# Optimization experiments

Measured on AMD Instinct MI355X. Metric: run time of the kernel, lower is better.

Reference implementation:

```python
import jax, jax.numpy as jnp
import numpy as np

N_HEAD = 16
BLOCK_SIZE = 2049  # w2 last dim = block_size - 1 = 2048


def setup_inputs() -> dict:
    key = jax.random.key(0)
    ks = jax.random.split(key, 9)
    B, T, C = 2, 2048, 1024
    hd = C // N_HEAD
    M = BLOCK_SIZE - 1
    return {
        "x": jax.random.normal(ks[0], (B, T, C), jnp.float32),
        "w1_w": jax.random.normal(ks[1], (C, C), jnp.float32) * 0.02,
        "w1_b": jax.random.normal(ks[2], (C,), jnp.float32) * 0.02,
        # torch uniform_(a=-0.001, b=0.001)
        "w2": jax.random.uniform(ks[3], (N_HEAD, hd, M), jnp.float32, -0.001, 0.001),
        "b2": jax.random.normal(ks[4], (M,), jnp.float32) * 0.02,
        "value_w": jax.random.normal(ks[5], (C, C), jnp.float32) * 0.02,
        "value_b": jax.random.normal(ks[6], (C,), jnp.float32) * 0.02,
        "proj_w": jax.random.normal(ks[7], (C, C), jnp.float32) * 0.02,
        "proj_b": jax.random.normal(ks[8], (C,), jnp.float32) * 0.02,
    }


def reference(x, w1_w, w1_b, w2, b2, value_w, value_b, proj_w, proj_b):
    B, T, C = x.shape
    H = N_HEAD
    hd = C // H
    M = w2.shape[-1]  # block_size - 1
    # kernel = relu(w1(x)), split heads -> [B, H, T, hd]
    k = jax.nn.relu(x @ w1_w.T + w1_b).reshape(B, T, H, hd).transpose(0, 2, 1, 3)
    # synthesizer scores: [B, H, T, M]
    attn = jnp.einsum('bhtd,hdm->bhtm', k, w2) + b2
    # causal mask = tril(ones(block,block))[:T, :M] == 0 -> -inf
    causal = jnp.tril(jnp.ones((T, M), dtype=bool))
    attn = jnp.where(causal, attn, -jnp.inf)
    # softmax over first T score columns
    attn = jax.nn.softmax(attn[..., :T], axis=-1)  # [B, H, T, T]
    v = (x @ value_w.T + value_b).reshape(B, T, H, hd).transpose(0, 2, 1, 3)
    out = jnp.einsum('bhts,bhsd->bhtd', attn, v)
    out = out.transpose(0, 2, 1, 3).reshape(B, T, C)
    return out @ proj_w.T + proj_b
```

## Files before the change

### kernel.cpp

```cpp
#include <hip/hip_runtime.h>
#include <math.h>
#include <stdint.h>

typedef __bf16 bf16;
typedef __bf16 bf16x8 __attribute__((ext_vector_type(8)));
typedef __bf16 bf16x4 __attribute__((ext_vector_type(4)));
typedef float f32x4 __attribute__((ext_vector_type(4)));
typedef float f32x16 __attribute__((ext_vector_type(16)));
typedef unsigned int u32;

__device__ __forceinline__ int swz(int row, int chunk) {
    return row * 64 + ((chunk ^ (row & 7)) << 3);
}

__device__ __forceinline__ void gld16(void* lds, const void* g) {
    __builtin_amdgcn_global_load_lds(
        (const __attribute__((address_space(1))) u32*)g,
        (__attribute__((address_space(3))) u32*)lds, 16, 0, 0);
}

__global__ void cast_bf16_k(const float* __restrict__ src, bf16* __restrict__ dst, int n) {
    const int stride = gridDim.x * blockDim.x * 4;
    for (int i = (blockIdx.x * blockDim.x + threadIdx.x) * 4; i < n; i += stride) {
        float4 v = *(const float4*)(src + i);
        bf16x4 o = {(bf16)v.x, (bf16)v.y, (bf16)v.z, (bf16)v.w};
        *(bf16x4*)(dst + i) = o;
    }
}

__global__ void cast3_bf16_k(const float* __restrict__ s0, bf16* __restrict__ d0,
                             const float* __restrict__ s1, bf16* __restrict__ d1,
                             const float* __restrict__ s2, bf16* __restrict__ d2, int n) {
    const int stride = gridDim.x * blockDim.x * 4;
    for (int i = (blockIdx.x * blockDim.x + threadIdx.x) * 4; i < n; i += stride) {
        float4 v0 = *(const float4*)(s0 + i);
        float4 v1 = *(const float4*)(s1 + i);
        float4 v2 = *(const float4*)(s2 + i);
        bf16x4 o0 = {(bf16)v0.x, (bf16)v0.y, (bf16)v0.z, (bf16)v0.w};
        bf16x4 o1 = {(bf16)v1.x, (bf16)v1.y, (bf16)v1.z, (bf16)v1.w};
        bf16x4 o2 = {(bf16)v2.x, (bf16)v2.y, (bf16)v2.z, (bf16)v2.w};
        *(bf16x4*)(d0 + i) = o0;
        *(bf16x4*)(d1 + i) = o1;
        *(bf16x4*)(d2 + i) = o2;
    }
}

__global__ __launch_bounds__(256) void w2_transpose_k(const float* __restrict__ w2,
                                                      bf16* __restrict__ w2t, int M) {
    __shared__ float Tf[64][65];
    const int h = blockIdx.y, m0 = blockIdx.x * 64, t = threadIdx.x;
    {
        const int dr = t >> 4, c4 = (t & 15) * 4;
        #pragma unroll
        for (int it = 0; it < 4; ++it) {
            const int d = dr + it * 16;
            float4 v = *(const float4*)(w2 + ((size_t)h * 64 + d) * M + m0 + c4);
            Tf[d][c4] = v.x; Tf[d][c4 + 1] = v.y; Tf[d][c4 + 2] = v.z; Tf[d][c4 + 3] = v.w;
        }
    }
    __syncthreads();
    const int m = t >> 2;
    #pragma unroll
    for (int it = 0; it < 2; ++it) {
        const int ch = (t & 3) + it * 4;
        bf16x8 o;
        #pragma unroll
        for (int j = 0; j < 8; ++j) o[j] = (bf16)Tf[ch * 8 + j][m];
        *(bf16x8*)(w2t + ((size_t)h * M + m0 + m) * 64 + ch * 8) = o;
    }
}

__global__ __launch_bounds__(256, 2) void gemm_bf16_k(const bf16* __restrict__ A,
                                                   const bf16* __restrict__ Bw,
                                                   const float* __restrict__ bias,
                                                   const float* __restrict__ bias2,
                                                   float* __restrict__ C0,
                                                   bf16* __restrict__ CK,
                                                   bf16* __restrict__ CV,
                                                   int M, int N, int K, int mode, int Ns)
{
    __shared__ __align__(16) bf16 As[2][128 * 64];
    __shared__ __align__(16) bf16 Bs[2][128 * 64];
    const int tid = threadIdx.x;
    const int w = tid >> 6, l = tid & 63;
    const int wr = w >> 1, wc = w & 1;
    const int lc = l & 15, lg = l >> 4;
    const int row0 = blockIdx.y * 128, col0 = blockIdx.x * 128;

    f32x4 acc[4][4] = {};

    const int nk = K >> 6;
    auto issue = [&](int buf, int k0) {
        #pragma unroll
        for (int i = 0; i < 4; ++i) {
            const int br = (w * 4 + i) * 8;
            const int r = br + (l >> 3);
            const int gs = (l & 7) ^ (r & 7);
            gld16(&As[buf][br * 64], A  + (size_t)(row0 + r) * K + k0 + gs * 8);
            gld16(&Bs[buf][br * 64], Bw + (size_t)(col0 + r) * K + k0 + gs * 8);
        }
    };

    issue(0, 0);
    int cur = 0;
    for (int kt = 0; kt < nk; ++kt) {
        if (kt + 1 < nk) {
            issue(cur ^ 1, (kt + 1) << 6);
            asm volatile("s_waitcnt vmcnt(8)" ::: "memory");
        } else {
            asm volatile("s_waitcnt vmcnt(0)" ::: "memory");
        }
        __builtin_amdgcn_s_barrier();
        #pragma unroll
        for (int ks = 0; ks < 2; ++ks) {
            bf16x8 af[4], bfv[4];
            #pragma unroll
            for (int i = 0; i < 4; ++i) {
                af[i]  = *(const bf16x8*)&As[cur][swz(wr * 64 + i * 16 + lc, ks * 4 + lg)];
                bfv[i] = *(const bf16x8*)&Bs[cur][swz(wc * 64 + i * 16 + lc, ks * 4 + lg)];
            }
            #pragma unroll
            for (int mi = 0; mi < 4; ++mi)
                #pragma unroll
                for (int ni = 0; ni < 4; ++ni)
                    acc[mi][ni] = __builtin_amdgcn_mfma_f32_16x16x32_bf16(af[mi], bfv[ni], acc[mi][ni], 0, 0, 0);
        }
        asm volatile("s_waitcnt lgkmcnt(0)" ::: "memory");
        __builtin_amdgcn_s_barrier();
        cur ^= 1;
    }

    #pragma unroll
    for (int ni = 0; ni < 4; ++ni) {
        const int col = col0 + wc * 64 + ni * 16 + lc;
        #pragma unroll
        for (int mi = 0; mi < 4; ++mi) {
            const int rowb = row0 + wr * 64 + mi * 16 + lg * 4;
            f32x4 v = acc[mi][ni];
            if (mode == 0) {
                const float bv = bias[col];
                #pragma unroll
                for (int r = 0; r < 4; ++r)
                    C0[(size_t)(rowb + r) * N + col] = v[r] + bv;
            } else if (col < Ns) {
                const float bv = bias[col];
                #pragma unroll
                for (int r = 0; r < 4; ++r)
                    CK[(size_t)(rowb + r) * Ns + col] = (bf16)fmaxf(v[r] + bv, 0.f);
            } else {
                const float bv = bias2[col - Ns];
                const int b = rowb >> 11, tt = rowb & 2047;
                bf16x4 o = {(bf16)(v[0] + bv), (bf16)(v[1] + bv),
                            (bf16)(v[2] + bv), (bf16)(v[3] + bv)};
                *(bf16x4*)(CV + ((size_t)b * Ns + (col - Ns)) * 2048 + tt) = o;
            }
        }
    }
}

__global__ __launch_bounds__(512, 4) void synth_attn_v11(const bf16* __restrict__ Kb,
                                                         const bf16* __restrict__ VT,
                                                         const bf16* __restrict__ w2t,
                                                         const float* __restrict__ b2,
                                                         bf16* __restrict__ Ob)
{
    constexpr int T = 2048, C = 1024, M = 2048;
    __shared__ __align__(16) bf16 ring[2][2][8192];
    __shared__ float b2l[M];
    const int tid = threadIdx.x;
    const int w = tid >> 6, l = tid & 63;
    const int c = l & 31, hi = l >> 5;
    const int sg = w & 1, qh = w >> 1;

    const int bx = blockIdx.x;
    const int u = bx & 255, rg = bx >> 8;
    const int t128 = rg ? (15 - (u & 15)) : (u & 15);
    const int bh = (u >> 4) + (rg << 4);
    const int h = bh & 15, b = bh >> 4;
    const int t0w = t128 * 128 + qh * 32;
    const int myT = 2 * t128 + (qh >> 1);

    *(float4*)&b2l[tid * 4] = *(const float4*)(b2 + tid * 4);
    __syncthreads();

    const bf16* Wg = w2t + (size_t)h * M * 64;
    const bf16* Vg = VT + ((size_t)b * C + h * 64) * T;

    const bf16* Kg = Kb + ((size_t)(b * T + t0w + c)) * C + h * 64 + hi * 8;
    bf16x8 kf[4];
    #pragma unroll
    for (int kst = 0; kst < 4; ++kst) kf[kst] = *(const bf16x8*)(Kg + kst * 16);

    auto stage = [&](int buf, int sb) {
        bf16* dst = &ring[sg][buf][0];
        const int s0 = sb * 64;
        const int jb = (qh & 1) * 4;
        if (qh < 2) {
            #pragma unroll
            for (int j = 0; j < 4; ++j) {
                const int jj = jb + j, r = jj >> 2, kst = jj & 3;
                gld16(dst + jj * 512,
                      Wg + ((size_t)(s0 + r * 32 + c)) * 64 + kst * 16 + hi * 8);
            }
        } else {
            #pragma unroll
            for (int j = 0; j < 4; ++j) {
                const int jj = jb + j, r = jj >> 2, m = jj & 3;
                gld16(dst + 4096 + jj * 512,
                      Vg + ((size_t)(r * 32 + c)) * T + s0 + m * 16 + hi * 8);
            }
        }
    };

    const int nIter = t128 + 1;
    stage(0, sg);

    f32x16 o0 = {}, o1 = {};
    float lsum = 0.f;

    for (int i = 0; i < nIter; ++i) {
        const int sb = 2 * i + sg;
        if (i + 1 < nIter) {
            stage((i + 1) & 1, sb + 2);
            asm volatile("s_waitcnt vmcnt(4)" ::: "memory");
        } else {
            asm volatile("s_waitcnt vmcnt(0)" ::: "memory");
        }
        __builtin_amdgcn_s_barrier();

        if (sb <= myT) {
            const bf16* Wb = &ring[sg][i & 1][0];
            const bf16* Vb = &ring[sg][i & 1][4096];
            const int s0 = sb * 64;

            f32x16 sv0, sv1;
            #pragma unroll
            for (int qd = 0; qd < 4; ++qd) {
                float4 b4 = *(const float4*)&b2l[s0 + qd * 8 + 4 * hi];
                float4 b5 = *(const float4*)&b2l[s0 + 32 + qd * 8 + 4 * hi];
                sv0[4*qd] = b4.x; sv0[4*qd+1] = b4.y; sv0[4*qd+2] = b4.z; sv0[4*qd+3] = b4.w;
                sv1[4*qd] = b5.x; sv1[4*qd+1] = b5.y; sv1[4*qd+2] = b5.z; sv1[4*qd+3] = b5.w;
            }
            #pragma unroll
            for (int kst = 0; kst < 4; ++kst) {
                bf16x8 w0 = *(const bf16x8*)&Wb[kst * 512 + l * 8];
                bf16x8 w1 = *(const bf16x8*)&Wb[(4 + kst) * 512 + l * 8];
                sv0 = __builtin_amdgcn_mfma_f32_32x32x16_bf16(w0, kf[kst], sv0, 0, 0, 0);
                sv1 = __builtin_amdgcn_mfma_f32_32x32x16_bf16(w1, kf[kst], sv1, 0, 0, 0);
            }

            const bool diag = (sb == myT);
            const int qv = (qh & 1) * 32 + c;
            u32 U0[8], U1[8];
            #pragma unroll
            for (int qd = 0; qd < 4; ++qd) {
                float e0[4], e1[4];
                #pragma unroll
                for (int k = 0; k < 4; ++k) {
                    const int sbase = qd * 8 + 4 * hi + k;
                    float ev0 = __expf(sv0[4*qd + k]);
                    float ev1 = __expf(sv1[4*qd + k]);
                    if (diag && sbase > qv)      ev0 = 0.f;
                    if (diag && sbase + 32 > qv) ev1 = 0.f;
                    lsum += ev0 + ev1;
                    e0[k] = ev0; e1[k] = ev1;
                }
                union { bf16x4 v; u32 uu[2]; } p0, p1;
                p0.v = {(bf16)e0[0], (bf16)e0[1], (bf16)e0[2], (bf16)e0[3]};
                p1.v = {(bf16)e1[0], (bf16)e1[1], (bf16)e1[2], (bf16)e1[3]};
                U0[2*qd] = p0.uu[0]; U0[2*qd+1] = p0.uu[1];
                U1[2*qd] = p1.uu[0]; U1[2*qd+1] = p1.uu[1];
            }

            #define PV_TILE(Uarr, st)                                              \
            {                                                                      \
                _Pragma("unroll")                                                  \
                for (int kk = 0; kk < 2; ++kk) {                                   \
                    u32 A00 = Uarr[4*kk],   A01 = Uarr[4*kk+1];                    \
                    u32 A10 = Uarr[4*kk+2], A11 = Uarr[4*kk+3];                    \
                    u32 s00 = (u32)__shfl_xor((int)A00, 32);                       \
                    u32 s01 = (u32)__shfl_xor((int)A01, 32);                       \
                    u32 s10 = (u32)__shfl_xor((int)A10, 32);                       \
                    u32 s11 = (u32)__shfl_xor((int)A11, 32);                       \
                    union { u32 uu[4]; bf16x8 v; } pa;                             \
                    pa.uu[0] = hi ? s10 : A00;                                     \
                    pa.uu[1] = hi ? s11 : A01;                                     \
                    pa.uu[2] = hi ? A10 : s00;                                     \
                    pa.uu[3] = hi ? A11 : s01;                                     \
                    const int m = (st) * 2 + kk;                                   \
                    bf16x8 v0 = *(const bf16x8*)&Vb[m * 512 + l * 8];              \
                    bf16x8 v1 = *(const bf16x8*)&Vb[(4 + m) * 512 + l * 8];        \
                    o0 = __builtin_amdgcn_mfma_f32_32x32x16_bf16(pa.v, v0, o0, 0, 0, 0); \
                    o1 = __builtin_amdgcn_mfma_f32_32x32x16_bf16(pa.v, v1, o1, 0, 0, 0); \
                }                                                                  \
            }
            PV_TILE(U0, 0)
            PV_TILE(U1, 1)
            #undef PV_TILE
        }

        asm volatile("s_waitcnt lgkmcnt(0)" ::: "memory");
        __builtin_amdgcn_s_barrier();
    }

    float* scr = (float*)&ring[0][0][0];
    float* base = scr + qh * 2112;
    if (sg == 1) {
        #pragma unroll
        for (int k = 0; k < 16; ++k) base[k * 64 + l] = o0[k];
        #pragma unroll
        for (int k = 0; k < 16; ++k) base[(16 + k) * 64 + l] = o1[k];
        base[32 * 64 + l] = lsum;
    }
    __syncthreads();
    if (sg == 0) {
        #pragma unroll
        for (int k = 0; k < 16; ++k) o0[k] += base[k * 64 + l];
        #pragma unroll
        for (int k = 0; k < 16; ++k) o1[k] += base[(16 + k) * 64 + l];
        lsum += base[32 * 64 + l];
        const float inv = 1.f / (lsum + __shfl_xor(lsum, 32));
        #pragma unroll
        for (int r = 0; r < 16; ++r) {
            const int q_ = (r & 3) + 8 * (r >> 2) + 4 * hi;
            const float iv = __shfl(inv, q_);
            bf16* dst = Ob + (size_t)(b * T + t0w + q_) * C + h * 64;
            dst[c]      = (bf16)(o0[r] * iv);
            dst[32 + c] = (bf16)(o1[r] * iv);
        }
    }
}

extern "C" void kernel_launch(void* const* d_in, const int* in_sizes, int n_in,
                              void* d_out, int out_size, void* d_ws, size_t ws_size,
                              hipStream_t stream) {
    const float* x       = (const float*)d_in[0];
    const float* w1_w    = (const float*)d_in[1];
    const float* w1_b    = (const float*)d_in[2];
    const float* w2      = (const float*)d_in[3];
    const float* b2      = (const float*)d_in[4];
    const float* value_w = (const float*)d_in[5];
    const float* value_b = (const float*)d_in[6];
    const float* proj_w  = (const float*)d_in[7];
    const float* proj_b  = (const float*)d_in[8];

    const int B = 2, T = 2048, C = 1024, H = 16, M = 2048;
    const int R = B * T;

    bf16* xb  = (bf16*)d_ws;
    bf16* w1b = xb  + (size_t)R * C;
    bf16* vwb = w1b + (size_t)C * C;
    bf16* w2t = vwb + (size_t)C * C;
    bf16* pwb = w2t + (size_t)H * M * 64;
    bf16* Kb  = pwb + (size_t)C * C;
    bf16* VTb = Kb  + (size_t)R * C;
    bf16* Ob  = VTb + (size_t)R * C;

    cast_bf16_k<<<1024, 256, 0, stream>>>(x, xb, R * C);
    cast3_bf16_k<<<512, 256, 0, stream>>>(w1_w, w1b, value_w, vwb, proj_w, pwb, C * C);
    w2_transpose_k<<<dim3(M / 64, H), 256, 0, stream>>>(w2, w2t, M);

    gemm_bf16_k<<<dim3(2 * C / 128, R / 128), 256, 0, stream>>>(
        xb, w1b, w1_b, value_b, nullptr, Kb, VTb, R, 2 * C, C, 1, C);

    synth_attn_v11<<<dim3(512), 512, 0, stream>>>(Kb, VTb, w2t, b2, Ob);

    gemm_bf16_k<<<dim3(C / 128, R / 128), 256, 0, stream>>>(
        Ob, pwb, proj_b, nullptr, (float*)d_out, nullptr, nullptr, R, C, C, 0, C);
}
```

Baseline: 109.9 us.

## Split attention over key-range chunks with atomic accumulation and separate normalize pass

Replaces the 512-thread blocks, which covered each query tile's full causal key range split between two wave groups, with 256-thread blocks that each handle up to 8 key tiles of one query tile. Later query tiles get more blocks, giving 1280 roughly balanced blocks. Partial outputs and row sums are combined with float atomicAdds into zeroed fp32 buffers, and a new kernel normalizes them and casts to bf16. The aim is better load balance and occupancy under the causal triangle. The cost is a memset, heavy global atomic traffic, an extra full-size fp32 read/write pass, and non-deterministic summation order.

```diff
diff --git a/kernel.cpp b/kernel.cpp
--- a/kernel.cpp
+++ b/kernel.cpp
@@ -158,30 +158,35 @@
     }
 }
 
-__global__ __launch_bounds__(512, 4) void synth_attn_v11(const bf16* __restrict__ Kb,
+__global__ __launch_bounds__(256, 4) void synth_attn_v12(const bf16* __restrict__ Kb,
                                                          const bf16* __restrict__ VT,
                                                          const bf16* __restrict__ w2t,
                                                          const float* __restrict__ b2,
-                                                         bf16* __restrict__ Ob)
+                                                         float* __restrict__ Oacc,
+                                                         float* __restrict__ Lacc)
 {
-    constexpr int T = 2048, C = 1024, M = 2048;
-    __shared__ __align__(16) bf16 ring[2][2][8192];
-    __shared__ float b2l[M];
+    constexpr int T = 2048, C = 1024, M = 2048, H = 16;
+    __shared__ __align__(16) bf16 ring[2][8192];
+    __shared__ float b2l[512];
     const int tid = threadIdx.x;
     const int w = tid >> 6, l = tid & 63;
     const int c = l & 31, hi = l >> 5;
-    const int sg = w & 1, qh = w >> 1;
 
     const int bx = blockIdx.x;
-    const int u = bx & 255, rg = bx >> 8;
-    const int t128 = rg ? (15 - (u & 15)) : (u & 15);
-    const int bh = (u >> 4) + (rg << 4);
+    const int bh = bx / 40, u = bx % 40;
+    int t, sp;
+    if (u < 4)       { t = u;                sp = 0; }
+    else if (u < 12) { t = 4 + ((u - 4) >> 1);  sp = (u - 4) & 1; }
+    else if (u < 24) { t = 8 + (u - 12) / 3;    sp = (u - 12) % 3; }
+    else             { t = 12 + ((u - 24) >> 2); sp = (u - 24) & 3; }
     const int h = bh & 15, b = bh >> 4;
-    const int t0w = t128 * 128 + qh * 32;
-    const int myT = 2 * t128 + (qh >> 1);
-
-    *(float4*)&b2l[tid * 4] = *(const float4*)(b2 + tid * 4);
-    __syncthreads();
+    const int t0w = t * 128 + w * 32;
+    const int myT = 2 * t + (w >> 1);
+    const int sLo = sp * 8;
+    const int nT = min(8, 2 * t + 2 - sLo);
+
+    *(float2*)&b2l[tid * 2] = *(const float2*)(b2 + sp * 512 + tid * 2);
+    asm volatile("s_waitcnt lgkmcnt(0)" ::: "memory");
 
     const bf16* Wg = w2t + (size_t)h * M * 64;
     const bf16* Vg = VT + ((size_t)b * C + h * 64) * T;
@@ -192,36 +197,28 @@
     for (int kst = 0; kst < 4; ++kst) kf[kst] = *(const bf16x8*)(Kg + kst * 16);
 
     auto stage = [&](int buf, int sb) {
-        bf16* dst = &ring[sg][buf][0];
+        bf16* dst = &ring[buf][0];
         const int s0 = sb * 64;
-        const int jb = (qh & 1) * 4;
-        if (qh < 2) {
-            #pragma unroll
-            for (int j = 0; j < 4; ++j) {
-                const int jj = jb + j, r = jj >> 2, kst = jj & 3;
-                gld16(dst + jj * 512,
-                      Wg + ((size_t)(s0 + r * 32 + c)) * 64 + kst * 16 + hi * 8);
-            }
-        } else {
-            #pragma unroll
-            for (int j = 0; j < 4; ++j) {
-                const int jj = jb + j, r = jj >> 2, m = jj & 3;
-                gld16(dst + 4096 + jj * 512,
-                      Vg + ((size_t)(r * 32 + c)) * T + s0 + m * 16 + hi * 8);
-            }
+        #pragma unroll
+        for (int j = 0; j < 2; ++j) {
+            const int jj = w * 2 + j;
+            const int r = jj >> 2, k4 = jj & 3;
+            gld16(dst + jj * 512,
+                  Wg + ((size_t)(s0 + r * 32 + c)) * 64 + k4 * 16 + hi * 8);
+            gld16(dst + 4096 + jj * 512,
+                  Vg + ((size_t)(r * 32 + c)) * T + s0 + k4 * 16 + hi * 8);
         }
     };
 
-    const int nIter = t128 + 1;
-    stage(0, sg);
+    stage(0, sLo);
 
     f32x16 o0 = {}, o1 = {};
     float lsum = 0.f;
 
-    for (int i = 0; i < nIter; ++i) {
-        const int sb = 2 * i + sg;
-        if (i + 1 < nIter) {
-            stage((i + 1) & 1, sb + 2);
+    for (int i = 0; i < nT; ++i) {
+        const int sb = sLo + i;
+        if (i + 1 < nT) {
+            stage((i + 1) & 1, sb + 1);
             asm volatile("s_waitcnt vmcnt(4)" ::: "memory");
         } else {
             asm volatile("s_waitcnt vmcnt(0)" ::: "memory");
@@ -229,15 +226,15 @@
         __builtin_amdgcn_s_barrier();
 
         if (sb <= myT) {
-            const bf16* Wb = &ring[sg][i & 1][0];
-            const bf16* Vb = &ring[sg][i & 1][4096];
-            const int s0 = sb * 64;
+            const bf16* Wb = &ring[i & 1][0];
+            const bf16* Vb = &ring[i & 1][4096];
+            const int s0l = sb * 64 - sp * 512;
 
             f32x16 sv0, sv1;
             #pragma unroll
             for (int qd = 0; qd < 4; ++qd) {
-                float4 b4 = *(const float4*)&b2l[s0 + qd * 8 + 4 * hi];
-                float4 b5 = *(const float4*)&b2l[s0 + 32 + qd * 8 + 4 * hi];
+                float4 b4 = *(const float4*)&b2l[s0l + qd * 8 + 4 * hi];
+                float4 b5 = *(const float4*)&b2l[s0l + 32 + qd * 8 + 4 * hi];
                 sv0[4*qd] = b4.x; sv0[4*qd+1] = b4.y; sv0[4*qd+2] = b4.z; sv0[4*qd+3] = b4.w;
                 sv1[4*qd] = b5.x; sv1[4*qd+1] = b5.y; sv1[4*qd+2] = b5.z; sv1[4*qd+3] = b5.w;
             }
@@ -250,7 +247,7 @@
             }
 
             const bool diag = (sb == myT);
-            const int qv = (qh & 1) * 32 + c;
+            const int qv = (w & 1) * 32 + c;
             u32 U0[8], U1[8];
             #pragma unroll
             for (int qd = 0; qd < 4; ++qd) {
@@ -303,32 +300,32 @@
         __builtin_amdgcn_s_barrier();
     }
 
-    float* scr = (float*)&ring[0][0][0];
-    float* base = scr + qh * 2112;
-    if (sg == 1) {
-        #pragma unroll
-        for (int k = 0; k < 16; ++k) base[k * 64 + l] = o0[k];
-        #pragma unroll
-        for (int k = 0; k < 16; ++k) base[(16 + k) * 64 + l] = o1[k];
-        base[32 * 64 + l] = lsum;
-    }
-    __syncthreads();
-    if (sg == 0) {
-        #pragma unroll
-        for (int k = 0; k < 16; ++k) o0[k] += base[k * 64 + l];
-        #pragma unroll
-        for (int k = 0; k < 16; ++k) o1[k] += base[(16 + k) * 64 + l];
-        lsum += base[32 * 64 + l];
-        const float inv = 1.f / (lsum + __shfl_xor(lsum, 32));
-        #pragma unroll
-        for (int r = 0; r < 16; ++r) {
-            const int q_ = (r & 3) + 8 * (r >> 2) + 4 * hi;
-            const float iv = __shfl(inv, q_);
-            bf16* dst = Ob + (size_t)(b * T + t0w + q_) * C + h * 64;
-            dst[c]      = (bf16)(o0[r] * iv);
-            dst[32 + c] = (bf16)(o1[r] * iv);
-        }
-    }
+    lsum += __shfl_xor(lsum, 32);
+    if (hi == 0)
+        atomicAdd(&Lacc[((size_t)(b * H + h)) * T + t0w + c], lsum);
+    #pragma unroll
+    for (int r = 0; r < 16; ++r) {
+        const int q_ = (r & 3) + 8 * (r >> 2) + 4 * hi;
+        float* p = Oacc + ((size_t)(b * T + t0w + q_)) * C + h * 64;
+        atomicAdd(p + c,      o0[r]);
+        atomicAdd(p + c + 32, o1[r]);
+    }
+}
+
+__global__ __launch_bounds__(256) void attn_norm_k(const float* __restrict__ Oacc,
+                                                   const float* __restrict__ Lacc,
+                                                   bf16* __restrict__ Ob)
+{
+    const int i = (blockIdx.x * blockDim.x + threadIdx.x) * 4;
+    const int row = i >> 10;
+    const int ch = i & 1023;
+    const int h = ch >> 6;
+    const int b = row >> 11, tq = row & 2047;
+    const float inv = 1.f / Lacc[((size_t)(b * 16 + h)) * 2048 + tq];
+    float4 v = *(const float4*)(Oacc + i);
+    bf16x4 o = {(bf16)(v.x * inv), (bf16)(v.y * inv),
+                (bf16)(v.z * inv), (bf16)(v.w * inv)};
+    *(bf16x4*)(Ob + i) = o;
 }
 
 extern "C" void kernel_launch(void* const* d_in, const int* in_sizes, int n_in,
@@ -355,6 +352,10 @@
     bf16* Kb  = pwb + (size_t)C * C;
     bf16* VTb = Kb  + (size_t)R * C;
     bf16* Ob  = VTb + (size_t)R * C;
+    float* Oacc = (float*)(Ob + (size_t)R * C);
+    float* Lacc = Oacc + (size_t)R * C;
+
+    hipMemsetAsync(Oacc, 0, ((size_t)R * C + (size_t)B * H * T) * sizeof(float), stream);
 
     cast_bf16_k<<<1024, 256, 0, stream>>>(x, xb, R * C);
     cast3_bf16_k<<<512, 256, 0, stream>>>(w1_w, w1b, value_w, vwb, proj_w, pwb, C * C);
@@ -363,7 +364,8 @@
     gemm_bf16_k<<<dim3(2 * C / 128, R / 128), 256, 0, stream>>>(
         xb, w1b, w1_b, value_b, nullptr, Kb, VTb, R, 2 * C, C, 1, C);
 
-    synth_attn_v11<<<dim3(512), 512, 0, stream>>>(Kb, VTb, w2t, b2, Ob);
+    synth_attn_v12<<<dim3(1280), 256, 0, stream>>>(Kb, VTb, w2t, b2, Oacc, Lacc);
+    attn_norm_k<<<dim3(R * C / 1024), 256, 0, stream>>>(Oacc, Lacc, Ob);
 
     gemm_bf16_k<<<dim3(C / 128, R / 128), 256, 0, stream>>>(
         Ob, pwb, proj_b, nullptr, (float*)d_out, nullptr, nullptr, R, C, C, 0, C);
```

Result: slower. 129.0 us (+17.4%).
